# Performance work log

Hardware: AMD Instinct MI355X
Metric: run time of the kernel (lower is better)

Reference implementation:

```python
import jax, jax.numpy as jnp
import numpy as np

IN_CH = 1
C = 128      # residual_channels
S = 128      # skip_channels
NUM_BLOCKS = 2
NUM_LAYERS = 10
DILATIONS = [2 ** d for _ in range(NUM_BLOCKS) for d in range(NUM_LAYERS)]  # len 20
L = len(DILATIONS)
B = 2
T = 8192


def setup_inputs() -> dict:
    key = jax.random.key(0)
    ks = jax.random.split(key, 12)
    sc = 0.1
    x = jax.random.normal(ks[0], (B, IN_CH, T), dtype=jnp.float32)
    w_in = jax.random.normal(ks[1], (C, IN_CH), dtype=jnp.float32) * sc
    b_in = jax.random.normal(ks[2], (C,), dtype=jnp.float32) * sc
    w_dil = jax.random.normal(ks[3], (L, C, C, 2), dtype=jnp.float32) * sc
    b_dil = jax.random.normal(ks[4], (L, C), dtype=jnp.float32) * sc
    w_tanh = jax.random.normal(ks[5], (L, C, C), dtype=jnp.float32) * sc
    b_tanh = jax.random.normal(ks[6], (L, C), dtype=jnp.float32) * sc
    w_sig = jax.random.normal(ks[7], (L, C, C), dtype=jnp.float32) * sc
    b_sig = jax.random.normal(ks[8], (L, C), dtype=jnp.float32) * sc
    w_skip = jax.random.normal(ks[9], (L, S, C), dtype=jnp.float32) * sc
    b_skip = jax.random.normal(ks[10], (L, S), dtype=jnp.float32) * sc
    return {"x": x, "w_in": w_in, "b_in": b_in, "w_dil": w_dil, "b_dil": b_dil,
            "w_tanh": w_tanh, "b_tanh": b_tanh, "w_sig": w_sig, "b_sig": b_sig,
            "w_skip": w_skip, "b_skip": b_skip}


def _conv1x1(w, b, x):
    # w: [O, C], x: [B, C, T] -> [B, O, T]
    return jnp.einsum('oc,bct->bot', w, x) + b[None, :, None]


def _dilated_conv_k2(w, b, x, d):
    # causal dilated conv, kernel_size=2: y[t] = w0 @ x[t-d] + w1 @ x[t]
    xp = jnp.pad(x, ((0, 0), (0, 0), (d, 0)))  # left causal pad
    y = (jnp.einsum('oc,bct->bot', w[:, :, 0], xp[:, :, :x.shape[-1]])
         + jnp.einsum('oc,bct->bot', w[:, :, 1], xp[:, :, d:]))
    return y + b[None, :, None]


def reference(x, w_in, b_in, w_dil, b_dil, w_tanh, b_tanh, w_sig, b_sig, w_skip, b_skip):
    h = _conv1x1(w_in, b_in, x)  # [B, C, T]
    outputs = []
    skips = []
    for i, d in enumerate(DILATIONS):
        outputs.append(h)
        x_dil = _dilated_conv_k2(w_dil[i], b_dil[i], h, d)
        x_filt = jnp.tanh(_conv1x1(w_tanh[i], b_tanh[i], x_dil))
        x_gate = jax.nn.sigmoid(_conv1x1(w_sig[i], b_sig[i], x_dil))
        x_h = x_gate * x_filt
        skips.append(_conv1x1(w_skip[i], b_skip[i], x_h))
        h = x_h + x_dil  # note: conv_residual is unused in the original forward
    return (jnp.stack(outputs, axis=0), jnp.stack(skips, axis=0))  # [L,B,C,T], [L,B,S,T]
```

## Files before the change

### kernel.cpp

```cpp
#include <hip/hip_runtime.h>
#include <math.h>


typedef _Float16 half8 __attribute__((ext_vector_type(8)));
typedef float floatx4 __attribute__((ext_vector_type(4)));
typedef float float4a __attribute__((ext_vector_type(4), aligned(4)));

namespace {
constexpr int C  = 128;
constexpr int S_ = 128;
constexpr int T  = 8192;
constexpr int B_ = 2;
constexpr int L_ = 20;
constexpr int NT = 64;
constexpr int P1 = 264;
constexpr int P2 = 136;
constexpr int DIL[L_] = {1,2,4,8,16,32,64,128,256,512,
                         1,2,4,8,16,32,64,128,256,512};
constexpr int WD_FRAG_L = 8 * 4 * 128;
constexpr int W1_FRAG_L = 4 * 4 * 128;
constexpr int NWD = L_ * WD_FRAG_L;
constexpr int NW1 = L_ * W1_FRAG_L;
}

__device__ __forceinline__ float fast_tanh(float x) { return 1.0f - 2.0f / (__expf(2.0f * x) + 1.0f); }
__device__ __forceinline__ float fast_sig (float x) { return 1.0f / (1.0f + __expf(-x)); }

__global__ __launch_bounds__(256) void prep_w(
    const float* __restrict__ wd, const float* __restrict__ wt,
    const float* __restrict__ wsg, const float* __restrict__ wk,
    _Float16* __restrict__ out)
{
    int fi = blockIdx.x * 256 + threadIdx.x;
    if (fi < NWD) {
        int i  = fi / WD_FRAG_L;
        int r  = fi % WD_FRAG_L;
        int kc = r >> 9;
        int q  = (r >> 7) & 3;
        int row = r & 127;
        int tap = kc >> 2;
        int ci0 = (kc & 3) * 32 + q * 8;
        const float* s = wd + ((size_t)(i * 128 + row) * 128 + ci0) * 2 + tap;
        half8 v;
#pragma unroll
        for (int j = 0; j < 8; ++j) v[j] = (_Float16)s[2 * j];
        *(half8*)(out + (size_t)fi * 8) = v;
        return;
    }
    int fi2 = fi - NWD;
    if (fi2 >= 3 * NW1) return;
    int mtx = fi2 / NW1;
    int r   = fi2 % NW1;
    int i   = r / W1_FRAG_L;
    int rr  = r % W1_FRAG_L;
    int kc  = rr >> 9;
    int q   = (rr >> 7) & 3;
    int row = rr & 127;
    const float* base = (mtx == 0) ? wt : ((mtx == 1) ? wsg : wk);
    const float* s = base + (size_t)(i * 128 + row) * 128 + kc * 32 + q * 8;
    half8 v;
#pragma unroll
    for (int j = 0; j < 8; ++j) v[j] = (_Float16)s[j];
    *(half8*)(out + (size_t)(NWD + fi2) * 8) = v;
}

__global__ __launch_bounds__(256) void in_conv(
    const float* __restrict__ x, const float* __restrict__ w_in,
    const float* __restrict__ b_in, float* __restrict__ h0)
{
    int idx = blockIdx.x * 256 + threadIdx.x;
    int t = idx & (T - 1);
    int c = (idx >> 13) & (C - 1);
    int b = idx >> 20;
    h0[idx] = w_in[c] * x[b * T + t] + b_in[c];
}

__global__ __launch_bounds__(256, 1) void layer_k(
    const float* __restrict__ h_in,
    float* __restrict__ h_out,
    float* __restrict__ skip_out,
    const _Float16* __restrict__ wd16, const float* __restrict__ bd,
    const _Float16* __restrict__ wt16, const float* __restrict__ bt,
    const _Float16* __restrict__ ws16, const float* __restrict__ bs,
    const _Float16* __restrict__ wk16, const float* __restrict__ bk,
    int d)
{
    __shared__ _Float16 sh[NT * P1];
    __shared__ _Float16 sx[NT * P2];
    _Float16* sxh = sh;

    const int tid = threadIdx.x;
    const int b   = blockIdx.y;
    const int t0  = blockIdx.x * NT;
    const float* hb = h_in + (size_t)b * C * T;

    for (int f = tid; f < C * (NT / 4); f += 256) {
        int ci = f >> 4, tq = f & 15;
        float4 v = *(const float4*)&hb[ci * T + t0 + tq * 4];
        _Float16* p = &sh[(tq * 4) * P1 + 128 + ci];
        p[0] = (_Float16)v.x; p[P1] = (_Float16)v.y;
        p[2 * P1] = (_Float16)v.z; p[3 * P1] = (_Float16)v.w;
    }
    for (int f = tid; f < C * (NT / 4); f += 256) {
        int ci = f >> 4, tq = f & 15;
        int ts = t0 + tq * 4 - d;
        float4 v;
        if (ts >= 0) {
            float4a u = *(const float4a*)&hb[ci * T + ts];
            v = make_float4(u.x, u.y, u.z, u.w);
        } else {
            v.x = 0.f;
            v.y = (ts + 1 >= 0) ? hb[ci * T + ts + 1] : 0.f;
            v.z = (ts + 2 >= 0) ? hb[ci * T + ts + 2] : 0.f;
            v.w = (ts + 3 >= 0) ? hb[ci * T + ts + 3] : 0.f;
        }
        _Float16* p = &sh[(tq * 4) * P1 + ci];
        p[0] = (_Float16)v.x; p[P1] = (_Float16)v.y;
        p[2 * P1] = (_Float16)v.z; p[3 * P1] = (_Float16)v.w;
    }
    __syncthreads();

    const int lane = tid & 63;
    const int wv   = tid >> 6;
    const int m16  = lane & 15;
    const int q    = lane >> 4;
    const int cb   = wv * 32;

    half8 wdf[2][8];
#pragma unroll
    for (int kc = 0; kc < 8; ++kc) {
        const _Float16* p = wd16 + (size_t)((kc * 4 + q) * 128) * 8;
#pragma unroll
        for (int mt = 0; mt < 2; ++mt)
            wdf[mt][kc] = *(const half8*)(p + (cb + mt * 16 + m16) * 8);
    }
    floatx4 bias_d[2];
#pragma unroll
    for (int mt = 0; mt < 2; ++mt)
#pragma unroll
        for (int r = 0; r < 4; ++r) bias_d[mt][r] = bd[cb + mt * 16 + q * 4 + r];

    floatx4 xdacc[2][4];
#pragma unroll
    for (int nt = 0; nt < 4; ++nt) {
        const _Float16* br = &sh[(nt * 16 + m16) * P1 + q * 8];
        half8 bf[8];
#pragma unroll
        for (int kc = 0; kc < 8; ++kc) bf[kc] = *(const half8*)(br + kc * 32);
#pragma unroll
        for (int mt = 0; mt < 2; ++mt) {
            floatx4 acc = bias_d[mt];
#pragma unroll
            for (int kc = 0; kc < 8; ++kc)
                acc = __builtin_amdgcn_mfma_f32_16x16x32_f16(wdf[mt][kc], bf[kc], acc, 0, 0, 0);
            xdacc[mt][nt] = acc;
            _Float16* px = &sx[(nt * 16 + m16) * P2 + cb + mt * 16 + q * 4];
#pragma unroll
            for (int r = 0; r < 4; ++r) px[r] = (_Float16)acc[r];
        }
    }
    __syncthreads();

    half8 wtf[2][4], wsf[2][4];
#pragma unroll
    for (int kc = 0; kc < 4; ++kc) {
        const size_t off = (size_t)((kc * 4 + q) * 128) * 8;
#pragma unroll
        for (int mt = 0; mt < 2; ++mt) {
            const int row = cb + mt * 16 + m16;
            wtf[mt][kc] = *(const half8*)(wt16 + off + row * 8);
            wsf[mt][kc] = *(const half8*)(ws16 + off + row * 8);
        }
    }
    floatx4 bias_t[2], bias_s[2];
#pragma unroll
    for (int mt = 0; mt < 2; ++mt)
#pragma unroll
        for (int r = 0; r < 4; ++r) {
            bias_t[mt][r] = bt[cb + mt * 16 + q * 4 + r];
            bias_s[mt][r] = bs[cb + mt * 16 + q * 4 + r];
        }

    float* ho = h_out ? h_out + (size_t)b * C * T : nullptr;
#pragma unroll
    for (int nt = 0; nt < 4; ++nt) {
        const _Float16* br = &sx[(nt * 16 + m16) * P2 + q * 8];
        half8 bf[4];
#pragma unroll
        for (int kc = 0; kc < 4; ++kc) bf[kc] = *(const half8*)(br + kc * 32);
#pragma unroll
        for (int mt = 0; mt < 2; ++mt) {
            floatx4 at = bias_t[mt], as = bias_s[mt];
#pragma unroll
            for (int kc = 0; kc < 4; ++kc) {
                at = __builtin_amdgcn_mfma_f32_16x16x32_f16(wtf[mt][kc], bf[kc], at, 0, 0, 0);
                as = __builtin_amdgcn_mfma_f32_16x16x32_f16(wsf[mt][kc], bf[kc], as, 0, 0, 0);
            }
            _Float16* pxh = &sxh[(nt * 16 + m16) * P2 + cb + mt * 16 + q * 4];
#pragma unroll
            for (int r = 0; r < 4; ++r) {
                float xh = fast_tanh(at[r]) * fast_sig(as[r]);
                pxh[r] = (_Float16)xh;
                if (ho)
                    ho[(size_t)(cb + mt * 16 + q * 4 + r) * T + t0 + nt * 16 + m16]
                        = xh + xdacc[mt][nt][r];
            }
        }
    }
    __syncthreads();

    half8 wkf[2][4];
#pragma unroll
    for (int kc = 0; kc < 4; ++kc) {
        const size_t off = (size_t)((kc * 4 + q) * 128) * 8;
#pragma unroll
        for (int mt = 0; mt < 2; ++mt)
            wkf[mt][kc] = *(const half8*)(wk16 + off + (cb + mt * 16 + m16) * 8);
    }
    floatx4 bias_k[2];
#pragma unroll
    for (int mt = 0; mt < 2; ++mt)
#pragma unroll
        for (int r = 0; r < 4; ++r) bias_k[mt][r] = bk[cb + mt * 16 + q * 4 + r];

    float* so = skip_out + (size_t)b * S_ * T;
#pragma unroll
    for (int nt = 0; nt < 4; ++nt) {
        const _Float16* br = &sxh[(nt * 16 + m16) * P2 + q * 8];
        half8 bf[4];
#pragma unroll
        for (int kc = 0; kc < 4; ++kc) bf[kc] = *(const half8*)(br + kc * 32);
#pragma unroll
        for (int mt = 0; mt < 2; ++mt) {
            floatx4 ak = bias_k[mt];
#pragma unroll
            for (int kc = 0; kc < 4; ++kc)
                ak = __builtin_amdgcn_mfma_f32_16x16x32_f16(wkf[mt][kc], bf[kc], ak, 0, 0, 0);
#pragma unroll
            for (int r = 0; r < 4; ++r)
                so[(size_t)(cb + mt * 16 + q * 4 + r) * T + t0 + nt * 16 + m16] = ak[r];
        }
    }
}

extern "C" void kernel_launch(void* const* d_in, const int* in_sizes, int n_in,
                              void* d_out, int out_size, void* d_ws, size_t ws_size,
                              hipStream_t stream)
{
    const float* x      = (const float*)d_in[0];
    const float* w_in   = (const float*)d_in[1];
    const float* b_in   = (const float*)d_in[2];
    const float* w_dil  = (const float*)d_in[3];
    const float* b_dil  = (const float*)d_in[4];
    const float* w_tanh = (const float*)d_in[5];
    const float* b_tanh = (const float*)d_in[6];
    const float* w_sig  = (const float*)d_in[7];
    const float* b_sig  = (const float*)d_in[8];
    const float* w_skip = (const float*)d_in[9];
    const float* b_skip = (const float*)d_in[10];

    float* outs  = (float*)d_out;
    float* skips = outs + (size_t)L_ * B_ * C * T;

    _Float16* w16   = (_Float16*)d_ws;
    _Float16* wd16  = w16;
    _Float16* wt16  = w16 + (size_t)NWD * 8;
    _Float16* wsg16 = wt16 + (size_t)NW1 * 8;
    _Float16* wk16  = wsg16 + (size_t)NW1 * 8;

    const int total_frags = NWD + 3 * NW1;
    prep_w<<<dim3((total_frags + 255) / 256), dim3(256), 0, stream>>>(
        w_dil, w_tanh, w_sig, w_skip, w16);

    in_conv<<<dim3(B_ * C * T / 256), dim3(256), 0, stream>>>(x, w_in, b_in, outs);

    for (int i = 0; i < L_; ++i) {
        const float* h_in  = outs + (size_t)i * B_ * C * T;
        float* h_out = (i + 1 < L_) ? outs + (size_t)(i + 1) * B_ * C * T : nullptr;
        float* sk_o  = skips + (size_t)i * B_ * S_ * T;
        layer_k<<<dim3(T / NT, B_), dim3(256), 0, stream>>>(
            h_in, h_out, sk_o,
            wd16  + (size_t)i * WD_FRAG_L * 8, b_dil  + (size_t)i * C,
            wt16  + (size_t)i * W1_FRAG_L * 8, b_tanh + (size_t)i * C,
            wsg16 + (size_t)i * W1_FRAG_L * 8, b_sig  + (size_t)i * C,
            wk16  + (size_t)i * W1_FRAG_L * 8, b_skip + (size_t)i * C,
            DIL[i]);
    }
}
```

Baseline: 628.5 us.

## Double layer kernel threads to 512, splitting time columns across wave pairs

The layer kernel now runs 512 threads per block. The 8 waves split as 4 channel groups by 2 time halves, so each wave handles 32 of the 64 time columns instead of all 64. This halves per-wave MFMA and epilogue work and raises the number of waves per CU. The cost is that each wave still loads the full weight fragments, so weight register and cache traffic per block doubles, and register pressure is tighter under launch bounds (512, 2).

```diff
diff --git a/kernel.cpp b/kernel.cpp
--- a/kernel.cpp
+++ b/kernel.cpp
@@ -13,6 +13,7 @@
 constexpr int B_ = 2;
 constexpr int L_ = 20;
 constexpr int NT = 64;
+constexpr int NTH = 512;
 constexpr int P1 = 264;
 constexpr int P2 = 136;
 constexpr int DIL[L_] = {1,2,4,8,16,32,64,128,256,512,
@@ -75,7 +76,7 @@
     h0[idx] = w_in[c] * x[b * T + t] + b_in[c];
 }
 
-__global__ __launch_bounds__(256, 1) void layer_k(
+__global__ __launch_bounds__(NTH, 2) void layer_k(
     const float* __restrict__ h_in,
     float* __restrict__ h_out,
     float* __restrict__ skip_out,
@@ -94,14 +95,14 @@
     const int t0  = blockIdx.x * NT;
     const float* hb = h_in + (size_t)b * C * T;
 
-    for (int f = tid; f < C * (NT / 4); f += 256) {
+    for (int f = tid; f < C * (NT / 4); f += NTH) {
         int ci = f >> 4, tq = f & 15;
         float4 v = *(const float4*)&hb[ci * T + t0 + tq * 4];
         _Float16* p = &sh[(tq * 4) * P1 + 128 + ci];
         p[0] = (_Float16)v.x; p[P1] = (_Float16)v.y;
         p[2 * P1] = (_Float16)v.z; p[3 * P1] = (_Float16)v.w;
     }
-    for (int f = tid; f < C * (NT / 4); f += 256) {
+    for (int f = tid; f < C * (NT / 4); f += NTH) {
         int ci = f >> 4, tq = f & 15;
         int ts = t0 + tq * 4 - d;
         float4 v;
@@ -122,9 +123,12 @@
 
     const int lane = tid & 63;
     const int wv   = tid >> 6;
+    const int wc   = wv & 3;
+    const int th   = wv >> 2;
     const int m16  = lane & 15;
     const int q    = lane >> 4;
-    const int cb   = wv * 32;
+    const int cb   = wc * 32;
+    const int tw   = th * 32;
 
     half8 wdf[2][8];
 #pragma unroll
@@ -140,10 +144,11 @@
 #pragma unroll
         for (int r = 0; r < 4; ++r) bias_d[mt][r] = bd[cb + mt * 16 + q * 4 + r];
 
-    floatx4 xdacc[2][4];
-#pragma unroll
-    for (int nt = 0; nt < 4; ++nt) {
-        const _Float16* br = &sh[(nt * 16 + m16) * P1 + q * 8];
+    floatx4 xdacc[2][2];
+#pragma unroll
+    for (int nt = 0; nt < 2; ++nt) {
+        const int rt = tw + nt * 16 + m16;
+        const _Float16* br = &sh[rt * P1 + q * 8];
         half8 bf[8];
 #pragma unroll
         for (int kc = 0; kc < 8; ++kc) bf[kc] = *(const half8*)(br + kc * 32);
@@ -154,7 +159,7 @@
             for (int kc = 0; kc < 8; ++kc)
                 acc = __builtin_amdgcn_mfma_f32_16x16x32_f16(wdf[mt][kc], bf[kc], acc, 0, 0, 0);
             xdacc[mt][nt] = acc;
-            _Float16* px = &sx[(nt * 16 + m16) * P2 + cb + mt * 16 + q * 4];
+            _Float16* px = &sx[rt * P2 + cb + mt * 16 + q * 4];
 #pragma unroll
             for (int r = 0; r < 4; ++r) px[r] = (_Float16)acc[r];
         }
@@ -183,8 +188,9 @@
 
     float* ho = h_out ? h_out + (size_t)b * C * T : nullptr;
 #pragma unroll
-    for (int nt = 0; nt < 4; ++nt) {
-        const _Float16* br = &sx[(nt * 16 + m16) * P2 + q * 8];
+    for (int nt = 0; nt < 2; ++nt) {
+        const int rt = tw + nt * 16 + m16;
+        const _Float16* br = &sx[rt * P2 + q * 8];
         half8 bf[4];
 #pragma unroll
         for (int kc = 0; kc < 4; ++kc) bf[kc] = *(const half8*)(br + kc * 32);
@@ -196,13 +202,13 @@
                 at = __builtin_amdgcn_mfma_f32_16x16x32_f16(wtf[mt][kc], bf[kc], at, 0, 0, 0);
                 as = __builtin_amdgcn_mfma_f32_16x16x32_f16(wsf[mt][kc], bf[kc], as, 0, 0, 0);
             }
-            _Float16* pxh = &sxh[(nt * 16 + m16) * P2 + cb + mt * 16 + q * 4];
+            _Float16* pxh = &sxh[rt * P2 + cb + mt * 16 + q * 4];
 #pragma unroll
             for (int r = 0; r < 4; ++r) {
                 float xh = fast_tanh(at[r]) * fast_sig(as[r]);
                 pxh[r] = (_Float16)xh;
                 if (ho)
-                    ho[(size_t)(cb + mt * 16 + q * 4 + r) * T + t0 + nt * 16 + m16]
+                    ho[(size_t)(cb + mt * 16 + q * 4 + r) * T + t0 + rt]
                         = xh + xdacc[mt][nt][r];
             }
         }
@@ -225,8 +231,9 @@
 
     float* so = skip_out + (size_t)b * S_ * T;
 #pragma unroll
-    for (int nt = 0; nt < 4; ++nt) {
-        const _Float16* br = &sxh[(nt * 16 + m16) * P2 + q * 8];
+    for (int nt = 0; nt < 2; ++nt) {
+        const int rt = tw + nt * 16 + m16;
+        const _Float16* br = &sxh[rt * P2 + q * 8];
         half8 bf[4];
 #pragma unroll
         for (int kc = 0; kc < 4; ++kc) bf[kc] = *(const half8*)(br + kc * 32);
@@ -238,7 +245,7 @@
                 ak = __builtin_amdgcn_mfma_f32_16x16x32_f16(wkf[mt][kc], bf[kc], ak, 0, 0, 0);
 #pragma unroll
             for (int r = 0; r < 4; ++r)
-                so[(size_t)(cb + mt * 16 + q * 4 + r) * T + t0 + nt * 16 + m16] = ak[r];
+                so[(size_t)(cb + mt * 16 + q * 4 + r) * T + t0 + rt] = ak[r];
         }
     }
 }
@@ -278,7 +285,7 @@
         const float* h_in  = outs + (size_t)i * B_ * C * T;
         float* h_out = (i + 1 < L_) ? outs + (size_t)(i + 1) * B_ * C * T : nullptr;
         float* sk_o  = skips + (size_t)i * B_ * S_ * T;
-        layer_k<<<dim3(T / NT, B_), dim3(256), 0, stream>>>(
+        layer_k<<<dim3(T / NT, B_), dim3(NTH), 0, stream>>>(
             h_in, h_out, sk_o,
             wd16  + (size_t)i * WD_FRAG_L * 8, b_dil  + (size_t)i * C,
             wt16  + (size_t)i * W1_FRAG_L * 8, b_tanh + (size_t)i * C,
```

Result: faster. 572.4 us (-8.9%).
